# Kernel optimization log

Hardware: AMD Instinct MI355X
Metric: run time of the kernel (lower is better)

Reference implementation:

```python
import jax, jax.numpy as jnp
import numpy as np

K = 9          # kernel_size (search window)
PAD = 4        # padding = (K-1)//2

def setup_inputs() -> dict:
    key = jax.random.key(0)
    k1, k2 = jax.random.split(key)
    B, C, H, W = 16, 512, 38, 68
    feat1 = jax.random.normal(k1, (B, C, H, W), dtype=jnp.float32)
    feat2 = jax.random.normal(k2, (B, C, H, W), dtype=jnp.float32)
    return {"feat1": feat1, "feat2": feat2}

def reference(feat1, feat2):
    # corr[b,c,k,h,w] = feat1[b,c,h,w] * feat2_pad[b,c,h+dy,w+dx]; output = max over the
    # K*K window offsets k. We compute the max incrementally over the 81 fixed offsets
    # instead of materializing the [B,C,81,H,W] unfold tensor (same math, less memory).
    B, C, H, W = feat1.shape
    f2 = jnp.pad(feat2, ((0, 0), (0, 0), (PAD, PAD), (PAD, PAD)))
    out = None
    for dy in range(K):
        for dx in range(K):
            corr = feat1 * f2[:, :, dy:dy + H, dx:dx + W]  # [B,C,H,W]
            out = corr if out is None else jnp.maximum(out, corr)
    return out
```

## Files before the change

kernel.cpp:

```cpp
#include <hip/hip_runtime.h>


#define HH 38
#define WW 68
#define PLANE (HH * WW)
#define ST 84
#define TPB 384
#define NB (16 * 512)

#define BAR() do { asm volatile("s_waitcnt lgkmcnt(0)" ::: "memory"); \
                   __builtin_amdgcn_s_barrier();                      \
                   __builtin_amdgcn_sched_barrier(0); } while (0)

__global__ __launch_bounds__(TPB) void corr_vh4_kernel(
    const float* __restrict__ f1, const float* __restrict__ f2,
    float* __restrict__ out)
{
    __shared__ float hmx[HH * ST];
    __shared__ float hmn[HH * ST];

    const int t = threadIdx.x;
    const int base = blockIdx.x * PLANE;
    const float* __restrict__ f2p = f2 + base;

    const int hr = t / 9, hs = t % 9;
    const int hc0 = (hs < 8) ? hs * 8 : 60;

    float4 fa, fb;
    if (t < 342) {
        fa = *reinterpret_cast<const float4*>(f1 + base + hr * WW + hc0);
        fb = *reinterpret_cast<const float4*>(f1 + base + hr * WW + hc0 + 4);
    }

    if (t < 152) {
        int row = t >> 2, q = t & 3;
        float* pl = (q & 2) ? hmn : hmx;
        *reinterpret_cast<float4*>(pl + row * ST + ((q & 1) ? 72 : 0)) =
            make_float4(0, 0, 0, 0);
    }

    if (t < 136) {
        const int cp = t % 34, seg = t / 34;
        const int c2 = cp * 2;
        const int h0 = (seg == 3) ? 28 : seg * 10;
        float2 v[18];
        #pragma unroll
        for (int i = 0; i < 18; ++i) {
            int row = h0 - 4 + i;
            v[i] = (row >= 0 && row < HH)
                 ? *reinterpret_cast<const float2*>(f2p + row * WW + c2)
                 : make_float2(0.0f, 0.0f);
        }
        float2 Sx[9], Sn[9];
        Sx[8] = v[8]; Sn[8] = v[8];
        #pragma unroll
        for (int i = 7; i >= 0; --i) {
            Sx[i] = make_float2(fmaxf(v[i].x, Sx[i+1].x), fmaxf(v[i].y, Sx[i+1].y));
            Sn[i] = make_float2(fminf(v[i].x, Sn[i+1].x), fminf(v[i].y, Sn[i+1].y));
        }
        *reinterpret_cast<float2*>(&hmx[h0 * ST + 4 + c2]) = Sx[0];
        *reinterpret_cast<float2*>(&hmn[h0 * ST + 4 + c2]) = Sn[0];
        float2 Px = v[9], Pn = v[9];
        #pragma unroll
        for (int k = 1; k <= 8; ++k) {
            *reinterpret_cast<float2*>(&hmx[(h0 + k) * ST + 4 + c2]) =
                make_float2(fmaxf(Sx[k].x, Px.x), fmaxf(Sx[k].y, Px.y));
            *reinterpret_cast<float2*>(&hmn[(h0 + k) * ST + 4 + c2]) =
                make_float2(fminf(Sn[k].x, Pn.x), fminf(Sn[k].y, Pn.y));
            if (k < 8) {
                Px = make_float2(fmaxf(Px.x, v[9 + k].x), fmaxf(Px.y, v[9 + k].y));
                Pn = make_float2(fminf(Pn.x, v[9 + k].x), fminf(Pn.y, v[9 + k].y));
            }
        }
        Px = make_float2(fmaxf(Px.x, v[17].x), fmaxf(Px.y, v[17].y));
        Pn = make_float2(fminf(Pn.x, v[17].x), fminf(Pn.y, v[17].y));
        *reinterpret_cast<float2*>(&hmx[(h0 + 9) * ST + 4 + c2]) = Px;
        *reinterpret_cast<float2*>(&hmn[(h0 + 9) * ST + 4 + c2]) = Pn;
    }

    BAR();

    if (t < 342) {
        float u[16], S[9], wx[8], wn[8], P;
        #pragma unroll
        for (int q = 0; q < 4; ++q)
            *reinterpret_cast<float4*>(&u[q * 4]) =
                *reinterpret_cast<const float4*>(&hmx[hr * ST + hc0 + q * 4]);
        S[8] = u[8];
        #pragma unroll
        for (int i = 7; i >= 0; --i) S[i] = fmaxf(u[i], S[i + 1]);
        wx[0] = S[0];
        P = u[9];
        #pragma unroll
        for (int k = 1; k < 8; ++k) {
            wx[k] = fmaxf(S[k], P);
            if (k < 7) P = fmaxf(P, u[9 + k]);
        }
        #pragma unroll
        for (int q = 0; q < 4; ++q)
            *reinterpret_cast<float4*>(&u[q * 4]) =
                *reinterpret_cast<const float4*>(&hmn[hr * ST + hc0 + q * 4]);
        S[8] = u[8];
        #pragma unroll
        for (int i = 7; i >= 0; --i) S[i] = fminf(u[i], S[i + 1]);
        wn[0] = S[0];
        P = u[9];
        #pragma unroll
        for (int k = 1; k < 8; ++k) {
            wn[k] = fminf(S[k], P);
            if (k < 7) P = fminf(P, u[9 + k]);
        }
        float4 ra, rb;
        ra.x = fa.x * (fa.x >= 0.0f ? wx[0] : wn[0]);
        ra.y = fa.y * (fa.y >= 0.0f ? wx[1] : wn[1]);
        ra.z = fa.z * (fa.z >= 0.0f ? wx[2] : wn[2]);
        ra.w = fa.w * (fa.w >= 0.0f ? wx[3] : wn[3]);
        rb.x = fb.x * (fb.x >= 0.0f ? wx[4] : wn[4]);
        rb.y = fb.y * (fb.y >= 0.0f ? wx[5] : wn[5]);
        rb.z = fb.z * (fb.z >= 0.0f ? wx[6] : wn[6]);
        rb.w = fb.w * (fb.w >= 0.0f ? wx[7] : wn[7]);
        *reinterpret_cast<float4*>(out + base + hr * WW + hc0)     = ra;
        *reinterpret_cast<float4*>(out + base + hr * WW + hc0 + 4) = rb;
    }
}

extern "C" void kernel_launch(void* const* d_in, const int* in_sizes, int n_in,
                              void* d_out, int out_size, void* d_ws, size_t ws_size,
                              hipStream_t stream) {
    const float* f1 = (const float*)d_in[0];
    const float* f2 = (const float*)d_in[1];
    float* out = (float*)d_out;
    corr_vh4_kernel<<<dim3(NB), dim3(TPB), 0, stream>>>(f1, f2, out);
}
```

Measured before the change: 46.03 us.

## Process two planes per block with all threads doing vertical pass

Each block now handles two channel planes, so the grid is halved. The vertical max/min pass is spread over 340 threads covering both planes, with 8-row segments instead of 136 threads doing 10-row segments. The horizontal pass loops over both planes, and the second plane's feat1 loads are issued after the barrier. The LDS row stride shrinks to 76 to make room for the doubled shared buffers. The aim is to raise thread utilisation in the vertical phase and add memory-level parallelism per block. In exchange, block count and occupancy headroom drop, and more loads are outstanding per thread.

```diff
diff --git a/kernel.cpp b/kernel.cpp
--- a/kernel.cpp
+++ b/kernel.cpp
@@ -4,123 +4,148 @@
 #define HH 38
 #define WW 68
 #define PLANE (HH * WW)
-#define ST 84
+#define ST 76
 #define TPB 384
-#define NB (16 * 512)
+#define PPB 2
+#define NB ((16 * 512) / PPB)
 
 #define BAR() do { asm volatile("s_waitcnt lgkmcnt(0)" ::: "memory"); \
                    __builtin_amdgcn_s_barrier();                      \
                    __builtin_amdgcn_sched_barrier(0); } while (0)
 
-__global__ __launch_bounds__(TPB) void corr_vh4_kernel(
+__device__ __forceinline__ float2 f2max(float2 a, float2 b) {
+    return make_float2(fmaxf(a.x, b.x), fmaxf(a.y, b.y));
+}
+__device__ __forceinline__ float2 f2min(float2 a, float2 b) {
+    return make_float2(fminf(a.x, b.x), fminf(a.y, b.y));
+}
+
+__global__ __launch_bounds__(TPB) void corr_ilp2_kernel(
     const float* __restrict__ f1, const float* __restrict__ f2,
     float* __restrict__ out)
 {
-    __shared__ float hmx[HH * ST];
-    __shared__ float hmn[HH * ST];
+    __shared__ float hmx[PPB][HH * ST];
+    __shared__ float hmn[PPB][HH * ST];
 
     const int t = threadIdx.x;
-    const int base = blockIdx.x * PLANE;
-    const float* __restrict__ f2p = f2 + base;
+    const int base0 = blockIdx.x * (PPB * PLANE);
 
     const int hr = t / 9, hs = t % 9;
     const int hc0 = (hs < 8) ? hs * 8 : 60;
+    const bool hAct = (t < 342);
 
-    float4 fa, fb;
-    if (t < 342) {
-        fa = *reinterpret_cast<const float4*>(f1 + base + hr * WW + hc0);
-        fb = *reinterpret_cast<const float4*>(f1 + base + hr * WW + hc0 + 4);
+    const int vp = t / 170, vj = t % 170;
+    const int vcp = vj % 34, vseg = vj / 34;
+    const int vc2 = vcp * 2;
+    const int vh0 = (vseg < 4) ? vseg * 8 : 30;
+    const bool vAct = (t < 340);
+
+    float2 v[16];
+    if (vAct) {
+        const float* fp = f2 + base0 + vp * PLANE;
+        #pragma unroll
+        for (int i = 0; i < 16; ++i) {
+            int row = vh0 - 4 + i;
+            v[i] = (row >= 0 && row < HH)
+                 ? *reinterpret_cast<const float2*>(fp + row * WW + vc2)
+                 : make_float2(0.0f, 0.0f);
+        }
     }
 
-    if (t < 152) {
-        int row = t >> 2, q = t & 3;
-        float* pl = (q & 2) ? hmn : hmx;
-        *reinterpret_cast<float4*>(pl + row * ST + ((q & 1) ? 72 : 0)) =
+    float4 fa0, fb0;
+    if (hAct) {
+        fa0 = *reinterpret_cast<const float4*>(f1 + base0 + hr * WW + hc0);
+        fb0 = *reinterpret_cast<const float4*>(f1 + base0 + hr * WW + hc0 + 4);
+    }
+
+    if (t < 304) {
+        int row = t >> 3, q = t & 7;
+        int side = q & 1, quant = (q >> 1) & 1, pl = q >> 2;
+        float* b = quant ? hmn[pl] : hmx[pl];
+        *reinterpret_cast<float4*>(b + row * ST + (side ? 72 : 0)) =
             make_float4(0, 0, 0, 0);
     }
 
-    if (t < 136) {
-        const int cp = t % 34, seg = t / 34;
-        const int c2 = cp * 2;
-        const int h0 = (seg == 3) ? 28 : seg * 10;
-        float2 v[18];
+    if (vAct) {
+        float* bx = hmx[vp];
+        float* bn = hmn[vp];
+        float2 S[9], P;
+        S[8] = v[8];
         #pragma unroll
-        for (int i = 0; i < 18; ++i) {
-            int row = h0 - 4 + i;
-            v[i] = (row >= 0 && row < HH)
-                 ? *reinterpret_cast<const float2*>(f2p + row * WW + c2)
-                 : make_float2(0.0f, 0.0f);
+        for (int i = 7; i >= 0; --i) S[i] = f2max(v[i], S[i + 1]);
+        *reinterpret_cast<float2*>(bx + vh0 * ST + 4 + vc2) = S[0];
+        P = v[9];
+        #pragma unroll
+        for (int k = 1; k < 8; ++k) {
+            *reinterpret_cast<float2*>(bx + (vh0 + k) * ST + 4 + vc2) = f2max(S[k], P);
+            if (k < 7) P = f2max(P, v[9 + k]);
         }
-        float2 Sx[9], Sn[9];
-        Sx[8] = v[8]; Sn[8] = v[8];
+        S[8] = v[8];
         #pragma unroll
-        for (int i = 7; i >= 0; --i) {
-            Sx[i] = make_float2(fmaxf(v[i].x, Sx[i+1].x), fmaxf(v[i].y, Sx[i+1].y));
-            Sn[i] = make_float2(fminf(v[i].x, Sn[i+1].x), fminf(v[i].y, Sn[i+1].y));
+        for (int i = 7; i >= 0; --i) S[i] = f2min(v[i], S[i + 1]);
+        *reinterpret_cast<float2*>(bn + vh0 * ST + 4 + vc2) = S[0];
+        P = v[9];
+        #pragma unroll
+        for (int k = 1; k < 8; ++k) {
+            *reinterpret_cast<float2*>(bn + (vh0 + k) * ST + 4 + vc2) = f2min(S[k], P);
+            if (k < 7) P = f2min(P, v[9 + k]);
         }
-        *reinterpret_cast<float2*>(&hmx[h0 * ST + 4 + c2]) = Sx[0];
-        *reinterpret_cast<float2*>(&hmn[h0 * ST + 4 + c2]) = Sn[0];
-        float2 Px = v[9], Pn = v[9];
-        #pragma unroll
-        for (int k = 1; k <= 8; ++k) {
-            *reinterpret_cast<float2*>(&hmx[(h0 + k) * ST + 4 + c2]) =
-                make_float2(fmaxf(Sx[k].x, Px.x), fmaxf(Sx[k].y, Px.y));
-            *reinterpret_cast<float2*>(&hmn[(h0 + k) * ST + 4 + c2]) =
-                make_float2(fminf(Sn[k].x, Pn.x), fminf(Sn[k].y, Pn.y));
-            if (k < 8) {
-                Px = make_float2(fmaxf(Px.x, v[9 + k].x), fmaxf(Px.y, v[9 + k].y));
-                Pn = make_float2(fminf(Pn.x, v[9 + k].x), fminf(Pn.y, v[9 + k].y));
-            }
-        }
-        Px = make_float2(fmaxf(Px.x, v[17].x), fmaxf(Px.y, v[17].y));
-        Pn = make_float2(fminf(Pn.x, v[17].x), fminf(Pn.y, v[17].y));
-        *reinterpret_cast<float2*>(&hmx[(h0 + 9) * ST + 4 + c2]) = Px;
-        *reinterpret_cast<float2*>(&hmn[(h0 + 9) * ST + 4 + c2]) = Pn;
     }
 
     BAR();
 
-    if (t < 342) {
-        float u[16], S[9], wx[8], wn[8], P;
-        #pragma unroll
-        for (int q = 0; q < 4; ++q)
-            *reinterpret_cast<float4*>(&u[q * 4]) =
-                *reinterpret_cast<const float4*>(&hmx[hr * ST + hc0 + q * 4]);
-        S[8] = u[8];
-        #pragma unroll
-        for (int i = 7; i >= 0; --i) S[i] = fmaxf(u[i], S[i + 1]);
-        wx[0] = S[0];
-        P = u[9];
-        #pragma unroll
-        for (int k = 1; k < 8; ++k) {
-            wx[k] = fmaxf(S[k], P);
-            if (k < 7) P = fmaxf(P, u[9 + k]);
+    float4 fa1, fb1;
+    if (hAct) {
+        fa1 = *reinterpret_cast<const float4*>(f1 + base0 + PLANE + hr * WW + hc0);
+        fb1 = *reinterpret_cast<const float4*>(f1 + base0 + PLANE + hr * WW + hc0 + 4);
+    }
+
+    #pragma unroll
+    for (int p = 0; p < PPB; ++p) {
+        if (hAct) {
+            float u[16], S[9], wx[8], wn[8], P;
+            #pragma unroll
+            for (int q = 0; q < 4; ++q)
+                *reinterpret_cast<float4*>(&u[q * 4]) =
+                    *reinterpret_cast<const float4*>(&hmx[p][hr * ST + hc0 + q * 4]);
+            S[8] = u[8];
+            #pragma unroll
+            for (int i = 7; i >= 0; --i) S[i] = fmaxf(u[i], S[i + 1]);
+            wx[0] = S[0];
+            P = u[9];
+            #pragma unroll
+            for (int k = 1; k < 8; ++k) {
+                wx[k] = fmaxf(S[k], P);
+                if (k < 7) P = fmaxf(P, u[9 + k]);
+            }
+            #pragma unroll
+            for (int q = 0; q < 4; ++q)
+                *reinterpret_cast<float4*>(&u[q * 4]) =
+                    *reinterpret_cast<const float4*>(&hmn[p][hr * ST + hc0 + q * 4]);
+            S[8] = u[8];
+            #pragma unroll
+            for (int i = 7; i >= 0; --i) S[i] = fminf(u[i], S[i + 1]);
+            wn[0] = S[0];
+            P = u[9];
+            #pragma unroll
+            for (int k = 1; k < 8; ++k) {
+                wn[k] = fminf(S[k], P);
+                if (k < 7) P = fminf(P, u[9 + k]);
+            }
+            float4 A = (p == 0) ? fa0 : fa1;
+            float4 B = (p == 0) ? fb0 : fb1;
+            float4 ra, rb;
+            ra.x = A.x * (A.x >= 0.0f ? wx[0] : wn[0]);
+            ra.y = A.y * (A.y >= 0.0f ? wx[1] : wn[1]);
+            ra.z = A.z * (A.z >= 0.0f ? wx[2] : wn[2]);
+            ra.w = A.w * (A.w >= 0.0f ? wx[3] : wn[3]);
+            rb.x = B.x * (B.x >= 0.0f ? wx[4] : wn[4]);
+            rb.y = B.y * (B.y >= 0.0f ? wx[5] : wn[5]);
+            rb.z = B.z * (B.z >= 0.0f ? wx[6] : wn[6]);
+            rb.w = B.w * (B.w >= 0.0f ? wx[7] : wn[7]);
+            *reinterpret_cast<float4*>(out + base0 + p * PLANE + hr * WW + hc0)     = ra;
+            *reinterpret_cast<float4*>(out + base0 + p * PLANE + hr * WW + hc0 + 4) = rb;
         }
-        #pragma unroll
-        for (int q = 0; q < 4; ++q)
-            *reinterpret_cast<float4*>(&u[q * 4]) =
-                *reinterpret_cast<const float4*>(&hmn[hr * ST + hc0 + q * 4]);
-        S[8] = u[8];
-        #pragma unroll
-        for (int i = 7; i >= 0; --i) S[i] = fminf(u[i], S[i + 1]);
-        wn[0] = S[0];
-        P = u[9];
-        #pragma unroll
-        for (int k = 1; k < 8; ++k) {
-            wn[k] = fminf(S[k], P);
-            if (k < 7) P = fminf(P, u[9 + k]);
-        }
-        float4 ra, rb;
-        ra.x = fa.x * (fa.x >= 0.0f ? wx[0] : wn[0]);
-        ra.y = fa.y * (fa.y >= 0.0f ? wx[1] : wn[1]);
-        ra.z = fa.z * (fa.z >= 0.0f ? wx[2] : wn[2]);
-        ra.w = fa.w * (fa.w >= 0.0f ? wx[3] : wn[3]);
-        rb.x = fb.x * (fb.x >= 0.0f ? wx[4] : wn[4]);
-        rb.y = fb.y * (fb.y >= 0.0f ? wx[5] : wn[5]);
-        rb.z = fb.z * (fb.z >= 0.0f ? wx[6] : wn[6]);
-        rb.w = fb.w * (fb.w >= 0.0f ? wx[7] : wn[7]);
-        *reinterpret_cast<float4*>(out + base + hr * WW + hc0)     = ra;
-        *reinterpret_cast<float4*>(out + base + hr * WW + hc0 + 4) = rb;
     }
 }
 
@@ -130,5 +155,5 @@
     const float* f1 = (const float*)d_in[0];
     const float* f2 = (const float*)d_in[1];
     float* out = (float*)d_out;
-    corr_vh4_kernel<<<dim3(NB), dim3(TPB), 0, stream>>>(f1, f2, out);
+    corr_ilp2_kernel<<<dim3(NB), dim3(TPB), 0, stream>>>(f1, f2, out);
 }
```

Result: faster. 45.10 us (-2.0%).
